# Kernel tuning notes

Measured on AMD Instinct MI355X. Metric: run time of the kernel, lower is better.

Reference implementation:

```python
import jax, jax.numpy as jnp
import numpy as np

G_DIMS = [30, 30, 24, 18, 18]
G_DOWN = [10, 10, 8, 6, 6]
S_DIM = 10
N_OBJ = 45
N_STREAMS = 5
P_DIM = sum(G_DOWN) * S_DIM          # 400
HID = 20 * S_DIM                     # 200
FREQS = np.array([0.01, 0.7, 0.91, 0.97, 0.99], dtype=np.float32)
DECAY, N_ITERS = 0.8, 5
HEB_LR, HEB_FORGET = 0.5, 0.9999
LOGSIG_RATIO, LOGSIG_OFFSET = 6.0, -2.0
B, T = 256, 8
_G_OFFS = np.concatenate([[0], np.cumsum(G_DIMS)]).astype(int)


def _leaky_clamp(x):
    # f(clamp(x, -1, 1)) with f = leaky_relu (torch default slope 0.01)
    return jax.nn.leaky_relu(jnp.clip(x, -1.0, 1.0))


def _scale_log_sigma(raw, temp=1.0):
    return LOGSIG_OFFSET + temp * jnp.tanh(raw / LOGSIG_RATIO) * LOGSIG_RATIO


def _downsample(g):  # [B, 120] -> [B, 40]; take first g_down dims of each stream
    return jnp.concatenate([g[:, o:o + d] for o, d in zip(_G_OFFS[:-1], G_DOWN)], axis=1)


def setup_inputs() -> dict:
    key = jax.random.key(0)
    ks = jax.random.split(key, 10)
    return {
        "g_seq": jax.random.normal(ks[0], (B, T, sum(G_DIMS)), jnp.float32),
        "x_idx": jax.random.randint(ks[1], (B, T), 0, N_OBJ),
        "W_comp": jax.random.normal(ks[2], (N_OBJ, S_DIM), jnp.float32) * 0.3,
        "W_repeat": jax.random.normal(ks[3], (P_DIM, sum(G_DOWN)), jnp.float32) * 0.2,
        "W_tile": jax.random.normal(ks[4], (P_DIM, N_STREAMS * S_DIM), jnp.float32) * 0.2,
        "W_tile0": jax.random.normal(ks[5], (G_DOWN[0] * S_DIM, S_DIM), jnp.float32) * 0.2,
        "w_x": jnp.ones((), jnp.float32),
        "b_x": jnp.zeros((S_DIM,), jnp.float32),
        "W1": jax.random.normal(ks[6], (S_DIM, HID), jnp.float32) * 0.2,
        "b1": jnp.zeros((HID,), jnp.float32),
        "W2": jax.random.normal(ks[7], (HID, N_OBJ), jnp.float32) * 0.1,
        "b2": jnp.zeros((N_OBJ,), jnp.float32),
        "W_lv1": jax.random.normal(ks[8], (P_DIM, P_DIM), jnp.float32) * 0.05,
        "b_lv1": jnp.zeros((P_DIM,), jnp.float32),
        "W_lv2": jax.random.normal(ks[9], (P_DIM, P_DIM), jnp.float32) * 0.05,
        "b_lv2": jnp.zeros((P_DIM,), jnp.float32),
    }


def _forward(g_seq, x_onehot, W_comp, W_repeat, W_tile, W_tile0, w_x, b_x,
             W1, b1, W2, b2, W_lv1, b_lv1, W_lv2, b_lv2):
    Bn = g_seq.shape[0]
    freqs = jnp.asarray(FREQS, dtype=g_seq.dtype)

    def step(carry, xs):
        M, x_filt = carry            # M: [B,P,P] Hebbian memory; x_filt: [B,5,10]
        g_t, x_t = xs                # g_t: [B,120], x_t: [B,45]
        # sensory compression + per-stream exponential temporal filtering
        x_c = x_t @ W_comp                                          # [B,10]
        x_filt = (1.0 - freqs)[None, :, None] * x_filt + freqs[None, :, None] * x_c[:, None, :]
        x_flat = x_filt.reshape(Bn, N_STREAMS * S_DIM)              # [B,50]
        # fused p-vector formation (_scriptable_fused_form_p)
        g_down = _downsample(g_t)                                   # [B,40]
        g_exp = g_down @ W_repeat.T                                 # [B,400]
        x_exp = x_flat @ W_tile.T                                   # [B,400]
        p_inf = _leaky_clamp(g_exp * x_exp)
        # attractor retrieval seeded from g projected to p-space (_scriptable_transform_g_to_p)
        h = _leaky_clamp(g_exp)
        for _ in range(N_ITERS):                                    # memory_iterations
            h = _leaky_clamp(DECAY * h + jnp.einsum('bij,bj->bi', M, h))
        p_ret = h
        # precision-weighted Gaussian fusion of inference and memory estimates
        lv1 = _scale_log_sigma(p_inf @ W_lv1 + b_lv1)
        lv2 = _scale_log_sigma(p_ret @ W_lv2 + b_lv2)
        inv1, inv2 = jnp.exp(-lv1), jnp.exp(-lv2)
        var_c = 1.0 / (inv1 + inv2)
        p_t = var_c * (p_inf * inv1 + p_ret * inv2)
        # Hebbian update: M <- lambda*M + eta*(p - p_hat)(p + p_hat)^T
        M = HEB_FORGET * M + HEB_LR * jnp.einsum('bi,bj->bij', p_t - p_ret, p_t + p_ret)
        # generative decode from stream-0 slice of p (GenerativeNetwork.forward_decode)
        x_s = w_x * (p_t[:, :G_DOWN[0] * S_DIM] @ W_tile0) + b_x    # [B,10]
        logits = jax.nn.elu(x_s @ W1 + b1) @ W2 + b2                # [B,45]
        return (M, x_filt), logits

    M0 = jnp.zeros((Bn, P_DIM, P_DIM), g_seq.dtype)
    xf0 = jnp.zeros((Bn, N_STREAMS, S_DIM), g_seq.dtype)
    xs = (jnp.swapaxes(g_seq, 0, 1), jnp.swapaxes(x_onehot, 0, 1))
    _, logits = jax.lax.scan(step, (M0, xf0), xs)                   # [T,B,45]
    return jnp.swapaxes(logits, 0, 1)                               # [B,T,45]


def reference(g_seq, x_idx, W_comp, W_repeat, W_tile, W_tile0, w_x, b_x,
              W1, b1, W2, b2, W_lv1, b_lv1, W_lv2, b_lv2):
    x_onehot = jax.nn.one_hot(x_idx, N_OBJ, dtype=g_seq.dtype)
    return _forward(g_seq, x_onehot, W_comp, W_repeat, W_tile, W_tile0, w_x, b_x,
                    W1, b1, W2, b2, W_lv1, b_lv1, W_lv2, b_lv2)
```

## Files before the change

kernel.cpp:

```cpp
#include <hip/hip_runtime.h>

#define kT 8
#define kG 120
#define kP 400
#define kObj 45
#define kS 10
#define kHid 200
#define NL 12
#define NV 24
#define NC (NL + NV)

__device__ __constant__ int c_gmap[40] = {
    0,1,2,3,4,5,6,7,8,9,
    30,31,32,33,34,35,36,37,38,39,
    60,61,62,63,64,65,66,67,
    84,85,86,87,88,89,
    102,103,104,105,106,107};

__device__ __constant__ float c_freq[5] = {0.01f, 0.7f, 0.91f, 0.97f, 0.99f};

__device__ __forceinline__ float leaky_clamp(float x) {
    x = fminf(fmaxf(x, -1.0f), 1.0f);
    return x > 0.0f ? x : 0.01f * x;
}

__global__ __launch_bounds__(512, 1) void tem_kernel(
    const float* __restrict__ g_seq, const int* __restrict__ x_idx,
    const float* __restrict__ W_comp, const float* __restrict__ W_repeat,
    const float* __restrict__ W_tile, const float* __restrict__ W_tile0,
    const float* __restrict__ w_x, const float* __restrict__ b_x,
    const float* __restrict__ W1, const float* __restrict__ b1,
    const float* __restrict__ W2, const float* __restrict__ b2,
    const float* __restrict__ W_lv1, const float* __restrict__ b_lv1,
    const float* __restrict__ W_lv2, const float* __restrict__ b_lv2,
    float* __restrict__ out)
{
    const int b   = blockIdx.x;
    const int tid = threadIdx.x;
    const int dim = tid;
    const bool hasD = (tid < kP);
    const int wid  = tid >> 6;
    const int lane = tid & 63;
    const int g   = tid >> 7;
    const int r   = tid & 127;
    const bool mact = (r < 100);

    const int phase = blockIdx.x >> 3;
    const int q   = (g + phase) & 3;
    const int qj0 = q * 100;
    const int soff = (phase * 2) & 63;
    const int joff = (phase * 13) % kP;

    __shared__ __align__(16) float pT[kP][kT];
    __shared__ __align__(16) float hT[kP][kT];
    __shared__ __align__(16) float lvT[kP][kT];
    __shared__ __align__(16) float xfT[50][kT];
    __shared__ __align__(16) float gdT[40][kT];
    __shared__ __align__(16) float s_wc[4][NL][kP];
    __shared__ float s_h[kP];
    __shared__ float s_u[kT][kP];
    __shared__ float s_v[kT][kP];
    __shared__ __align__(16) float s_part[4][kP];
    __shared__ float s_red[2][kT][8];
    __shared__ int   s_idx[kT];

    const float blv1 = hasD ? b_lv1[dim] : 0.0f;
    const float blv2 = hasD ? b_lv2[dim] : 0.0f;
    const float wx   = w_x[0];

    if (tid < kT) s_idx[tid] = x_idx[b * kT + tid];
    __syncthreads();

    if (mact) {
        #pragma unroll
        for (int k = 0; k < NL; ++k)
            ((float4*)&s_wc[g][k][0])[r] =
                ((const float4*)(W_lv2 + (qj0 + k) * kP))[r];
    }

    if (tid < 40) {
        int gi = c_gmap[tid];
        #pragma unroll
        for (int t = 0; t < kT; ++t)
            gdT[tid][t] = g_seq[(b * kT + t) * kG + gi];
    } else if (tid >= 64 && tid < 114) {
        int rr = tid - 64, d = rr % 10;
        float f = c_freq[rr / 10];
        float xf = 0.0f;
        #pragma unroll
        for (int t = 0; t < kT; ++t) {
            float xc = W_comp[s_idx[t] * kS + d];
            xf = (1.0f - f) * xf + f * xc;
            xfT[rr][t] = xf;
        }
    }
    __syncthreads();

    if (hasD) {
        float ge[kT], xe[kT];
        #pragma unroll
        for (int t = 0; t < kT; ++t) { ge[t] = 0.0f; xe[t] = 0.0f; }
        for (int j = 0; j < 40; ++j) {
            float w = W_repeat[dim * 40 + j];
            float4 gA = *(const float4*)&gdT[j][0];
            float4 gB = *(const float4*)&gdT[j][4];
            ge[0] += w * gA.x; ge[1] += w * gA.y; ge[2] += w * gA.z; ge[3] += w * gA.w;
            ge[4] += w * gB.x; ge[5] += w * gB.y; ge[6] += w * gB.z; ge[7] += w * gB.w;
        }
        for (int j = 0; j < 50; ++j) {
            float w = W_tile[dim * 50 + j];
            float4 xA = *(const float4*)&xfT[j][0];
            float4 xB = *(const float4*)&xfT[j][4];
            xe[0] += w * xA.x; xe[1] += w * xA.y; xe[2] += w * xA.z; xe[3] += w * xA.w;
            xe[4] += w * xB.x; xe[5] += w * xB.y; xe[6] += w * xB.z; xe[7] += w * xB.w;
        }
        float4 pA, pB, hA, hB;
        pA.x = leaky_clamp(ge[0] * xe[0]); pA.y = leaky_clamp(ge[1] * xe[1]);
        pA.z = leaky_clamp(ge[2] * xe[2]); pA.w = leaky_clamp(ge[3] * xe[3]);
        pB.x = leaky_clamp(ge[4] * xe[4]); pB.y = leaky_clamp(ge[5] * xe[5]);
        pB.z = leaky_clamp(ge[6] * xe[6]); pB.w = leaky_clamp(ge[7] * xe[7]);
        hA.x = leaky_clamp(ge[0]); hA.y = leaky_clamp(ge[1]);
        hA.z = leaky_clamp(ge[2]); hA.w = leaky_clamp(ge[3]);
        hB.x = leaky_clamp(ge[4]); hB.y = leaky_clamp(ge[5]);
        hB.z = leaky_clamp(ge[6]); hB.w = leaky_clamp(ge[7]);
        *(float4*)&pT[dim][0] = pA; *(float4*)&pT[dim][4] = pB;
        *(float4*)&hT[dim][0] = hA; *(float4*)&hT[dim][4] = hB;
    }
    __syncthreads();

    if (hasD) {
        float acc[kT];
        #pragma unroll
        for (int t = 0; t < kT; ++t) acc[t] = 0.0f;
        #pragma unroll 4
        for (int j = joff; j < kP; ++j) {
            float w = W_lv1[j * kP + dim];
            float4 pA = *(const float4*)&pT[j][0];
            float4 pB = *(const float4*)&pT[j][4];
            acc[0] += w * pA.x; acc[1] += w * pA.y; acc[2] += w * pA.z; acc[3] += w * pA.w;
            acc[4] += w * pB.x; acc[5] += w * pB.y; acc[6] += w * pB.z; acc[7] += w * pB.w;
        }
        #pragma unroll 4
        for (int j = 0; j < joff; ++j) {
            float w = W_lv1[j * kP + dim];
            float4 pA = *(const float4*)&pT[j][0];
            float4 pB = *(const float4*)&pT[j][4];
            acc[0] += w * pA.x; acc[1] += w * pA.y; acc[2] += w * pA.z; acc[3] += w * pA.w;
            acc[4] += w * pB.x; acc[5] += w * pB.y; acc[6] += w * pB.z; acc[7] += w * pB.w;
        }
        *(float4*)&lvT[dim][0] = make_float4(acc[0], acc[1], acc[2], acc[3]);
        *(float4*)&lvT[dim][4] = make_float4(acc[4], acc[5], acc[6], acc[7]);
    }
    __syncthreads();

    float4 wreg[NV];
    if (mact) {
        #pragma unroll
        for (int k = 0; k < NV; ++k)
            wreg[k] = ((const float4*)(W_lv2 + (qj0 + NL + k) * kP))[r];
    }

    int par = 0;
    for (int t = 0; t < kT; ++t) {
        float h = hasD ? hT[dim][t] : 0.0f;
        if (t == 0) {
            #pragma unroll
            for (int it = 0; it < 5; ++it) h = leaky_clamp(0.8f * h);
        } else {
            for (int it = 0; it < 5; ++it) {
                for (int s = 0; s < t; ++s) {
                    float p = hasD ? s_v[s][dim] * h : 0.0f;
                    #pragma unroll
                    for (int off = 32; off; off >>= 1) p += __shfl_down(p, off, 64);
                    if (lane == 0) s_red[par][s][wid] = p;
                }
                __syncthreads();
                if (hasD) {
                    float mh = 0.0f;
                    float c = 0.5f;
                    for (int s = t - 1; s >= 0; --s) {
                        float d = 0.0f;
                        #pragma unroll
                        for (int w = 0; w < 8; ++w) d += s_red[par][s][w];
                        mh += c * d * s_u[s][dim];
                        c *= 0.9999f;
                    }
                    h = leaky_clamp(0.8f * h + mh);
                }
                par ^= 1;
            }
        }
        if (hasD) s_h[dim] = h;
        __syncthreads();

        if (mact) {
            float4 a0{0,0,0,0}, a1{0,0,0,0}, a2{0,0,0,0}, a3{0,0,0,0};
            #pragma unroll
            for (int k = 0; k < NL; k += 4) {
                int j = qj0 + k;
                float4 w0 = ((const float4*)&s_wc[g][k+0][0])[r];
                float4 w1v = ((const float4*)&s_wc[g][k+1][0])[r];
                float4 w2v = ((const float4*)&s_wc[g][k+2][0])[r];
                float4 w3 = ((const float4*)&s_wc[g][k+3][0])[r];
                float v0 = s_h[j+0], v1 = s_h[j+1], v2 = s_h[j+2], v3 = s_h[j+3];
                a0.x += w0.x * v0; a0.y += w0.y * v0; a0.z += w0.z * v0; a0.w += w0.w * v0;
                a1.x += w1v.x * v1; a1.y += w1v.y * v1; a1.z += w1v.z * v1; a1.w += w1v.w * v1;
                a2.x += w2v.x * v2; a2.y += w2v.y * v2; a2.z += w2v.z * v2; a2.w += w2v.w * v2;
                a3.x += w3.x * v3; a3.y += w3.y * v3; a3.z += w3.z * v3; a3.w += w3.w * v3;
            }
            #pragma unroll
            for (int k = 0; k < NV; k += 4) {
                int j = qj0 + NL + k;
                float v0 = s_h[j+0], v1 = s_h[j+1], v2 = s_h[j+2], v3 = s_h[j+3];
                a0.x += wreg[k].x * v0; a0.y += wreg[k].y * v0; a0.z += wreg[k].z * v0; a0.w += wreg[k].w * v0;
                a1.x += wreg[k+1].x * v1; a1.y += wreg[k+1].y * v1; a1.z += wreg[k+1].z * v1; a1.w += wreg[k+1].w * v1;
                a2.x += wreg[k+2].x * v2; a2.y += wreg[k+2].y * v2; a2.z += wreg[k+2].z * v2; a2.w += wreg[k+2].w * v2;
                a3.x += wreg[k+3].x * v3; a3.y += wreg[k+3].y * v3; a3.z += wreg[k+3].z * v3; a3.w += wreg[k+3].w * v3;
            }
            #pragma unroll 4
            for (int jj = 0; jj < 64; jj += 2) {
                int j = qj0 + NC + ((jj + soff) & 63);
                float4 w0 = ((const float4*)(W_lv2 + (j+0) * kP))[r];
                float4 w1v = ((const float4*)(W_lv2 + (j+1) * kP))[r];
                float v0 = s_h[j+0], v1 = s_h[j+1];
                a0.x += w0.x * v0; a0.y += w0.y * v0; a0.z += w0.z * v0; a0.w += w0.w * v0;
                a1.x += w1v.x * v1; a1.y += w1v.y * v1; a1.z += w1v.z * v1; a1.w += w1v.w * v1;
            }
            float4 tot;
            tot.x = (a0.x + a1.x) + (a2.x + a3.x);
            tot.y = (a0.y + a1.y) + (a2.y + a3.y);
            tot.z = (a0.z + a1.z) + (a2.z + a3.z);
            tot.w = (a0.w + a1.w) + (a2.w + a3.w);
            ((float4*)&s_part[g][0])[r] = tot;
        }
        __syncthreads();

        if (hasD) {
            float lv2raw = (s_part[0][dim] + s_part[1][dim])
                         + (s_part[2][dim] + s_part[3][dim]) + blv2;
            float lv1raw = lvT[dim][t] + blv1;
            float l1 = -2.0f + 6.0f * tanhf(lv1raw * (1.0f / 6.0f));
            float l2 = -2.0f + 6.0f * tanhf(lv2raw * (1.0f / 6.0f));
            float i1v = expf(-l1), i2v = expf(-l2);
            float pinf = pT[dim][t];
            float p = (pinf * i1v + h * i2v) / (i1v + i2v);
            s_u[t][dim] = p - h;
            s_v[t][dim] = p + h;
        }
    }
    __syncthreads();

    float* dsc  = &hT[0][0];
    float* dhid = &lvT[0][0];

    if (tid < 480) {
        int t = tid / 60, rem = tid % 60;
        int d = rem / 6, k = rem % 6;
        int jlo = k * 17, jhi = (jlo + 17 > 100) ? 100 : jlo + 17;
        float acc = 0.0f;
        for (int j = jlo; j < jhi; ++j) {
            float pj = 0.5f * (s_u[t][j] + s_v[t][j]);
            acc += pj * W_tile0[j * kS + d];
        }
        dsc[(t * 10 + d) * 6 + k] = acc;
    }
    __syncthreads();
    if (tid < 80) {
        int t = tid / 10, d = tid % 10;
        float acc = 0.0f;
        #pragma unroll
        for (int k = 0; k < 6; ++k) acc += dsc[(t * 10 + d) * 6 + k];
        dsc[1000 + t * 10 + d] = wx * acc + b_x[d];
    }
    __syncthreads();
    for (int idx = tid; idx < kT * kHid; idx += 512) {
        int t = idx / kHid, hh = idx - t * kHid;
        float acc = b1[hh];
        #pragma unroll
        for (int d = 0; d < kS; ++d)
            acc += dsc[1000 + t * 10 + d] * W1[d * kHid + hh];
        dhid[t * kHid + hh] = acc > 0.0f ? acc : (expf(acc) - 1.0f);
    }
    __syncthreads();
    for (int idx = tid; idx < 720; idx += 512) {
        int t = idx / 90, rem = idx - t * 90;
        int half = rem / kObj, o = rem - half * kObj;
        int h0 = half * 100;
        float acc = 0.0f;
        for (int hh = h0; hh < h0 + 100; ++hh)
            acc += dhid[t * kHid + hh] * W2[hh * kObj + o];
        dsc[2000 + idx] = acc;
    }
    __syncthreads();
    if (tid < 360) {
        int t = tid / kObj, o = tid - t * kObj;
        out[(b * kT + t) * kObj + o] =
            b2[o] + dsc[2000 + t * 90 + o] + dsc[2000 + t * 90 + kObj + o];
    }
}

extern "C" void kernel_launch(void* const* d_in, const int* in_sizes, int n_in,
                              void* d_out, int out_size, void* d_ws, size_t ws_size,
                              hipStream_t stream) {
    const float* g_seq   = (const float*)d_in[0];
    const int*   x_idx   = (const int*)d_in[1];
    const float* W_comp  = (const float*)d_in[2];
    const float* W_repeat= (const float*)d_in[3];
    const float* W_tile  = (const float*)d_in[4];
    const float* W_tile0 = (const float*)d_in[5];
    const float* w_x     = (const float*)d_in[6];
    const float* b_x     = (const float*)d_in[7];
    const float* W1      = (const float*)d_in[8];
    const float* b1      = (const float*)d_in[9];
    const float* W2      = (const float*)d_in[10];
    const float* b2      = (const float*)d_in[11];
    const float* W_lv1   = (const float*)d_in[12];
    const float* b_lv1   = (const float*)d_in[13];
    const float* W_lv2   = (const float*)d_in[14];
    const float* b_lv2   = (const float*)d_in[15];
    float* out = (float*)d_out;

    const int Bn = in_sizes[0] / (kT * kG);
    tem_kernel<<<dim3(Bn), dim3(512), 0, stream>>>(
        g_seq, x_idx, W_comp, W_repeat, W_tile, W_tile0, w_x, b_x,
        W1, b1, W2, b2, W_lv1, b_lv1, W_lv2, b_lv2, out);
}
```

Before: 206.0 us.

## Double block to 1024 threads and split matvecs across more thread groups

Raises the block size from 512 to 1024 threads. The per-step W_lv2 matvec is now split over 8 row-slices of 50 rows instead of 4 slices of 100, so each thread keeps fewer cached weight rows in LDS and registers and streams a shorter tail per step. The W_lv1 precompute is split into two halves of the input dimension, combined through a shared buffer, and the decode reductions are spread over more threads. The aim is to shorten the serial per-timestep critical path with more parallel work. The cost is heavier barriers with 16 waves per block and extra partial-sum reductions.

```diff
diff --git a/kernel.cpp b/kernel.cpp
--- a/kernel.cpp
+++ b/kernel.cpp
@@ -6,9 +6,11 @@
 #define kObj 45
 #define kS 10
 #define kHid 200
-#define NL 12
-#define NV 24
-#define NC (NL + NV)
+#define NG 8
+#define SL 50
+#define NLr 4
+#define NVr 12
+#define NSr (SL - NLr - NVr)
 
 __device__ __constant__ int c_gmap[40] = {
     0,1,2,3,4,5,6,7,8,9,
@@ -24,7 +26,7 @@
     return x > 0.0f ? x : 0.01f * x;
 }
 
-__global__ __launch_bounds__(512, 1) void tem_kernel(
+__global__ __launch_bounds__(1024, 1) void tem_kernel(
     const float* __restrict__ g_seq, const int* __restrict__ x_idx,
     const float* __restrict__ W_comp, const float* __restrict__ W_repeat,
     const float* __restrict__ W_tile, const float* __restrict__ W_tile0,
@@ -41,26 +43,26 @@
     const bool hasD = (tid < kP);
     const int wid  = tid >> 6;
     const int lane = tid & 63;
-    const int g   = tid >> 7;
+    const int gg  = tid >> 7;
     const int r   = tid & 127;
     const bool mact = (r < 100);
 
     const int phase = blockIdx.x >> 3;
-    const int q   = (g + phase) & 3;
-    const int qj0 = q * 100;
-    const int soff = (phase * 2) & 63;
-    const int joff = (phase * 13) % kP;
+    const int ss  = (gg + phase) & 7;
+    const int sb  = ss * SL;
+    const int so  = phase % NSr;
+    const int joff = (phase * 13) % 200;
 
     __shared__ __align__(16) float pT[kP][kT];
     __shared__ __align__(16) float hT[kP][kT];
     __shared__ __align__(16) float lvT[kP][kT];
     __shared__ __align__(16) float xfT[50][kT];
     __shared__ __align__(16) float gdT[40][kT];
-    __shared__ __align__(16) float s_wc[4][NL][kP];
+    __shared__ __align__(16) float s_wc[NG][NLr][kP];
     __shared__ float s_h[kP];
     __shared__ float s_u[kT][kP];
     __shared__ float s_v[kT][kP];
-    __shared__ __align__(16) float s_part[4][kP];
+    __shared__ __align__(16) float s_part[NG][kP];
     __shared__ float s_red[2][kT][8];
     __shared__ int   s_idx[kT];
 
@@ -73,9 +75,9 @@
 
     if (mact) {
         #pragma unroll
-        for (int k = 0; k < NL; ++k)
-            ((float4*)&s_wc[g][k][0])[r] =
-                ((const float4*)(W_lv2 + (qj0 + k) * kP))[r];
+        for (int k = 0; k < NLr; ++k)
+            ((float4*)&s_wc[gg][k][0])[r] =
+                ((const float4*)(W_lv2 + (sb + k) * kP))[r];
     }
 
     if (tid < 40) {
@@ -128,36 +130,55 @@
     }
     __syncthreads();
 
-    if (hasD) {
+    {
+        const bool lvA = hasD;
+        const bool lvB = (tid >= 512 && tid < 912);
+        const int  ldim = lvA ? tid : (tid - 512);
         float acc[kT];
         #pragma unroll
         for (int t = 0; t < kT; ++t) acc[t] = 0.0f;
-        #pragma unroll 4
-        for (int j = joff; j < kP; ++j) {
-            float w = W_lv1[j * kP + dim];
-            float4 pA = *(const float4*)&pT[j][0];
-            float4 pB = *(const float4*)&pT[j][4];
-            acc[0] += w * pA.x; acc[1] += w * pA.y; acc[2] += w * pA.z; acc[3] += w * pA.w;
-            acc[4] += w * pB.x; acc[5] += w * pB.y; acc[6] += w * pB.z; acc[7] += w * pB.w;
-        }
-        #pragma unroll 4
-        for (int j = 0; j < joff; ++j) {
-            float w = W_lv1[j * kP + dim];
-            float4 pA = *(const float4*)&pT[j][0];
-            float4 pB = *(const float4*)&pT[j][4];
-            acc[0] += w * pA.x; acc[1] += w * pA.y; acc[2] += w * pA.z; acc[3] += w * pA.w;
-            acc[4] += w * pB.x; acc[5] += w * pB.y; acc[6] += w * pB.z; acc[7] += w * pB.w;
-        }
-        *(float4*)&lvT[dim][0] = make_float4(acc[0], acc[1], acc[2], acc[3]);
-        *(float4*)&lvT[dim][4] = make_float4(acc[4], acc[5], acc[6], acc[7]);
-    }
-    __syncthreads();
-
-    float4 wreg[NV];
+        if (lvA || lvB) {
+            const int jbase = lvA ? 0 : 200;
+            #pragma unroll 4
+            for (int jj = joff; jj < 200; ++jj) {
+                int j = jbase + jj;
+                float w = W_lv1[j * kP + ldim];
+                float4 pA = *(const float4*)&pT[j][0];
+                float4 pB = *(const float4*)&pT[j][4];
+                acc[0] += w * pA.x; acc[1] += w * pA.y; acc[2] += w * pA.z; acc[3] += w * pA.w;
+                acc[4] += w * pB.x; acc[5] += w * pB.y; acc[6] += w * pB.z; acc[7] += w * pB.w;
+            }
+            #pragma unroll 4
+            for (int jj = 0; jj < joff; ++jj) {
+                int j = jbase + jj;
+                float w = W_lv1[j * kP + ldim];
+                float4 pA = *(const float4*)&pT[j][0];
+                float4 pB = *(const float4*)&pT[j][4];
+                acc[0] += w * pA.x; acc[1] += w * pA.y; acc[2] += w * pA.z; acc[3] += w * pA.w;
+                acc[4] += w * pB.x; acc[5] += w * pB.y; acc[6] += w * pB.z; acc[7] += w * pB.w;
+            }
+        }
+        float* lv1b = &s_part[0][0];
+        if (lvB) {
+            ((float4*)lv1b)[ldim * 2 + 0] = make_float4(acc[0], acc[1], acc[2], acc[3]);
+            ((float4*)lv1b)[ldim * 2 + 1] = make_float4(acc[4], acc[5], acc[6], acc[7]);
+        }
+        __syncthreads();
+        if (hasD) {
+            float4 bA = ((float4*)lv1b)[dim * 2 + 0];
+            float4 bB = ((float4*)lv1b)[dim * 2 + 1];
+            *(float4*)&lvT[dim][0] =
+                make_float4(acc[0] + bA.x, acc[1] + bA.y, acc[2] + bA.z, acc[3] + bA.w);
+            *(float4*)&lvT[dim][4] =
+                make_float4(acc[4] + bB.x, acc[5] + bB.y, acc[6] + bB.z, acc[7] + bB.w);
+        }
+    }
+
+    float4 wreg[NVr];
     if (mact) {
         #pragma unroll
-        for (int k = 0; k < NV; ++k)
-            wreg[k] = ((const float4*)(W_lv2 + (qj0 + NL + k) * kP))[r];
+        for (int k = 0; k < NVr; ++k)
+            wreg[k] = ((const float4*)(W_lv2 + (sb + NLr + k) * kP))[r];
     }
 
     int par = 0;
@@ -168,11 +189,13 @@
             for (int it = 0; it < 5; ++it) h = leaky_clamp(0.8f * h);
         } else {
             for (int it = 0; it < 5; ++it) {
-                for (int s = 0; s < t; ++s) {
-                    float p = hasD ? s_v[s][dim] * h : 0.0f;
-                    #pragma unroll
-                    for (int off = 32; off; off >>= 1) p += __shfl_down(p, off, 64);
-                    if (lane == 0) s_red[par][s][wid] = p;
+                if (tid < 512) {
+                    for (int s = 0; s < t; ++s) {
+                        float p = hasD ? s_v[s][dim] * h : 0.0f;
+                        #pragma unroll
+                        for (int off = 32; off; off >>= 1) p += __shfl_down(p, off, 64);
+                        if (lane == 0) s_red[par][s][wid] = p;
+                    }
                 }
                 __syncthreads();
                 if (hasD) {
@@ -194,50 +217,45 @@
         __syncthreads();
 
         if (mact) {
-            float4 a0{0,0,0,0}, a1{0,0,0,0}, a2{0,0,0,0}, a3{0,0,0,0};
+            float4 a0{0,0,0,0}, a1{0,0,0,0};
             #pragma unroll
-            for (int k = 0; k < NL; k += 4) {
-                int j = qj0 + k;
-                float4 w0 = ((const float4*)&s_wc[g][k+0][0])[r];
-                float4 w1v = ((const float4*)&s_wc[g][k+1][0])[r];
-                float4 w2v = ((const float4*)&s_wc[g][k+2][0])[r];
-                float4 w3 = ((const float4*)&s_wc[g][k+3][0])[r];
-                float v0 = s_h[j+0], v1 = s_h[j+1], v2 = s_h[j+2], v3 = s_h[j+3];
+            for (int k = 0; k < NLr; k += 2) {
+                float4 w0 = ((const float4*)&s_wc[gg][k+0][0])[r];
+                float4 w1v = ((const float4*)&s_wc[gg][k+1][0])[r];
+                float v0 = s_h[sb+k+0], v1 = s_h[sb+k+1];
                 a0.x += w0.x * v0; a0.y += w0.y * v0; a0.z += w0.z * v0; a0.w += w0.w * v0;
                 a1.x += w1v.x * v1; a1.y += w1v.y * v1; a1.z += w1v.z * v1; a1.w += w1v.w * v1;
-                a2.x += w2v.x * v2; a2.y += w2v.y * v2; a2.z += w2v.z * v2; a2.w += w2v.w * v2;
-                a3.x += w3.x * v3; a3.y += w3.y * v3; a3.z += w3.z * v3; a3.w += w3.w * v3;
             }
             #pragma unroll
-            for (int k = 0; k < NV; k += 4) {
-                int j = qj0 + NL + k;
-                float v0 = s_h[j+0], v1 = s_h[j+1], v2 = s_h[j+2], v3 = s_h[j+3];
+            for (int k = 0; k < NVr; k += 2) {
+                float v0 = s_h[sb+NLr+k+0], v1 = s_h[sb+NLr+k+1];
                 a0.x += wreg[k].x * v0; a0.y += wreg[k].y * v0; a0.z += wreg[k].z * v0; a0.w += wreg[k].w * v0;
                 a1.x += wreg[k+1].x * v1; a1.y += wreg[k+1].y * v1; a1.z += wreg[k+1].z * v1; a1.w += wreg[k+1].w * v1;
-                a2.x += wreg[k+2].x * v2; a2.y += wreg[k+2].y * v2; a2.z += wreg[k+2].z * v2; a2.w += wreg[k+2].w * v2;
-                a3.x += wreg[k+3].x * v3; a3.y += wreg[k+3].y * v3; a3.z += wreg[k+3].z * v3; a3.w += wreg[k+3].w * v3;
-            }
+            }
+            const float* Wbase = W_lv2 + (sb + NLr + NVr) * kP;
             #pragma unroll 4
-            for (int jj = 0; jj < 64; jj += 2) {
-                int j = qj0 + NC + ((jj + soff) & 63);
-                float4 w0 = ((const float4*)(W_lv2 + (j+0) * kP))[r];
-                float4 w1v = ((const float4*)(W_lv2 + (j+1) * kP))[r];
-                float v0 = s_h[j+0], v1 = s_h[j+1];
+            for (int jj = 0; jj < NSr; jj += 2) {
+                int i0 = jj + so;     i0 -= (i0 >= NSr) ? NSr : 0;
+                int i1 = jj + 1 + so; i1 -= (i1 >= NSr) ? NSr : 0;
+                float4 w0 = ((const float4*)(Wbase + i0 * kP))[r];
+                float4 w1v = ((const float4*)(Wbase + i1 * kP))[r];
+                float v0 = s_h[sb + NLr + NVr + i0];
+                float v1 = s_h[sb + NLr + NVr + i1];
                 a0.x += w0.x * v0; a0.y += w0.y * v0; a0.z += w0.z * v0; a0.w += w0.w * v0;
                 a1.x += w1v.x * v1; a1.y += w1v.y * v1; a1.z += w1v.z * v1; a1.w += w1v.w * v1;
             }
             float4 tot;
-            tot.x = (a0.x + a1.x) + (a2.x + a3.x);
-            tot.y = (a0.y + a1.y) + (a2.y + a3.y);
-            tot.z = (a0.z + a1.z) + (a2.z + a3.z);
-            tot.w = (a0.w + a1.w) + (a2.w + a3.w);
-            ((float4*)&s_part[g][0])[r] = tot;
+            tot.x = a0.x + a1.x; tot.y = a0.y + a1.y;
+            tot.z = a0.z + a1.z; tot.w = a0.w + a1.w;
+            ((float4*)&s_part[gg][0])[r] = tot;
         }
         __syncthreads();
 
         if (hasD) {
-            float lv2raw = (s_part[0][dim] + s_part[1][dim])
-                         + (s_part[2][dim] + s_part[3][dim]) + blv2;
+            float lv2raw = ((s_part[0][dim] + s_part[1][dim])
+                          + (s_part[2][dim] + s_part[3][dim]))
+                         + ((s_part[4][dim] + s_part[5][dim])
+                          + (s_part[6][dim] + s_part[7][dim])) + blv2;
             float lv1raw = lvT[dim][t] + blv1;
             float l1 = -2.0f + 6.0f * tanhf(lv1raw * (1.0f / 6.0f));
             float l2 = -2.0f + 6.0f * tanhf(lv2raw * (1.0f / 6.0f));
@@ -253,43 +271,43 @@
     float* dsc  = &hT[0][0];
     float* dhid = &lvT[0][0];
 
-    if (tid < 480) {
-        int t = tid / 60, rem = tid % 60;
-        int d = rem / 6, k = rem % 6;
-        int jlo = k * 17, jhi = (jlo + 17 > 100) ? 100 : jlo + 17;
+    if (tid < 960) {
+        int t = tid / 120, rem = tid % 120;
+        int d = rem / 12, k = rem % 12;
+        int jlo = (k * 100) / 12, jhi = ((k + 1) * 100) / 12;
         float acc = 0.0f;
         for (int j = jlo; j < jhi; ++j) {
             float pj = 0.5f * (s_u[t][j] + s_v[t][j]);
             acc += pj * W_tile0[j * kS + d];
         }
-        dsc[(t * 10 + d) * 6 + k] = acc;
+        dsc[(t * 10 + d) * 12 + k] = acc;
     }
     __syncthreads();
     if (tid < 80) {
         int t = tid / 10, d = tid % 10;
         float acc = 0.0f;
         #pragma unroll
-        for (int k = 0; k < 6; ++k) acc += dsc[(t * 10 + d) * 6 + k];
-        dsc[1000 + t * 10 + d] = wx * acc + b_x[d];
-    }
-    __syncthreads();
-    for (int idx = tid; idx < kT * kHid; idx += 512) {
+        for (int k = 0; k < 12; ++k) acc += dsc[(t * 10 + d) * 12 + k];
+        dsc[1200 + t * 10 + d] = wx * acc + b_x[d];
+    }
+    __syncthreads();
+    for (int idx = tid; idx < kT * kHid; idx += 1024) {
         int t = idx / kHid, hh = idx - t * kHid;
         float acc = b1[hh];
         #pragma unroll
         for (int d = 0; d < kS; ++d)
-            acc += dsc[1000 + t * 10 + d] * W1[d * kHid + hh];
+            acc += dsc[1200 + t * 10 + d] * W1[d * kHid + hh];
         dhid[t * kHid + hh] = acc > 0.0f ? acc : (expf(acc) - 1.0f);
     }
     __syncthreads();
-    for (int idx = tid; idx < 720; idx += 512) {
-        int t = idx / 90, rem = idx - t * 90;
+    if (tid < 720) {
+        int t = tid / 90, rem = tid - t * 90;
         int half = rem / kObj, o = rem - half * kObj;
         int h0 = half * 100;
         float acc = 0.0f;
         for (int hh = h0; hh < h0 + 100; ++hh)
             acc += dhid[t * kHid + hh] * W2[hh * kObj + o];
-        dsc[2000 + idx] = acc;
+        dsc[2000 + tid] = acc;
     }
     __syncthreads();
     if (tid < 360) {
@@ -321,7 +339,7 @@
     float* out = (float*)d_out;
 
     const int Bn = in_sizes[0] / (kT * kG);
-    tem_kernel<<<dim3(Bn), dim3(512), 0, stream>>>(
+    tem_kernel<<<dim3(Bn), dim3(1024), 0, stream>>>(
         g_seq, x_idx, W_comp, W_repeat, W_tile, W_tile0, w_x, b_x,
         W1, b1, W2, b2, W_lv1, b_lv1, W_lv2, b_lv2, out);
 }
```

After: 208.7 us. No clear change (+1.3%).

## Double-buffer W_lv1 and W_lv2 streaming via async global-to-LDS loads

Applied to the files above, without the earlier changes.

Replaces direct per-thread global reads of W_lv1 and of the streamed part of W_lv2 with chunked, double-buffered async copies into LDS using global_load_lds. The persistent LDS cache of 12 W_lv2 rows is dropped, and each quarter keeps 24 rows in registers while the remaining 76 rows are staged per timestep in 13 chunks. The aim is to hide global-memory latency behind compute. In exchange it adds a block-wide barrier per chunk (25 for lv1, 13 per timestep for lv2) and a large LDS staging buffer.

```diff
diff --git a/kernel.cpp b/kernel.cpp
--- a/kernel.cpp
+++ b/kernel.cpp
@@ -6,9 +6,9 @@
 #define kObj 45
 #define kS 10
 #define kHid 200
-#define NL 12
 #define NV 24
-#define NC (NL + NV)
+#define NCH2 13
+#define NCH1 25
 
 __device__ __constant__ int c_gmap[40] = {
     0,1,2,3,4,5,6,7,8,9,
@@ -23,6 +23,23 @@
     x = fminf(fmaxf(x, -1.0f), 1.0f);
     return x > 0.0f ? x : 0.01f * x;
 }
+
+__device__ __forceinline__ void gl_lds16(const float* g, float* l) {
+    __builtin_amdgcn_global_load_lds(
+        (const __attribute__((address_space(1))) void*)g,
+        (__attribute__((address_space(3))) void*)l, 16, 0, 0);
+}
+
+__device__ __forceinline__ void stage(const float* g0, float* l0,
+                                      int nper, int lane) {
+    for (int k = 0; k < nper; k += 256) {
+        if (k + lane * 4 < nper)
+            gl_lds16(g0 + k + lane * 4, l0 + k);
+    }
+}
+
+__device__ __forceinline__ int ch_base(int c) { return c == 0 ? 0 : 4 + (c - 1) * 6; }
+__device__ __forceinline__ int ch_size(int c) { return c == 0 ? 4 : 6; }
 
 __global__ __launch_bounds__(512, 1) void tem_kernel(
     const float* __restrict__ g_seq, const int* __restrict__ x_idx,
@@ -35,34 +52,35 @@
     const float* __restrict__ W_lv2, const float* __restrict__ b_lv2,
     float* __restrict__ out)
 {
-    const int b   = blockIdx.x;
-    const int tid = threadIdx.x;
-    const int dim = tid;
+    const int b    = blockIdx.x;
+    const int tid  = threadIdx.x;
+    const int dim  = tid;
     const bool hasD = (tid < kP);
     const int wid  = tid >> 6;
+    const int widq = (tid >> 6) & 1;
     const int lane = tid & 63;
-    const int g   = tid >> 7;
-    const int r   = tid & 127;
+    const int g    = tid >> 7;
+    const int r    = tid & 127;
     const bool mact = (r < 100);
 
     const int phase = blockIdx.x >> 3;
-    const int q   = (g + phase) & 3;
-    const int qj0 = q * 100;
-    const int soff = (phase * 2) & 63;
-    const int joff = (phase * 13) % kP;
+    const int q    = (g + phase) & 3;
+    const int qj0  = q * 100;
+    const int coff  = phase % NCH2;
+    const int c1off = phase % NCH1;
 
     __shared__ __align__(16) float pT[kP][kT];
     __shared__ __align__(16) float hT[kP][kT];
     __shared__ __align__(16) float lvT[kP][kT];
     __shared__ __align__(16) float xfT[50][kT];
     __shared__ __align__(16) float gdT[40][kT];
-    __shared__ __align__(16) float s_wc[4][NL][kP];
-    __shared__ float s_h[kP];
+    __shared__ __align__(16) float s_h[kP];
     __shared__ float s_u[kT][kP];
     __shared__ float s_v[kT][kP];
     __shared__ __align__(16) float s_part[4][kP];
     __shared__ float s_red[2][kT][8];
     __shared__ int   s_idx[kT];
+    __shared__ __align__(16) float s_stg2[4][2][2400];
 
     const float blv1 = hasD ? b_lv1[dim] : 0.0f;
     const float blv2 = hasD ? b_lv2[dim] : 0.0f;
@@ -70,13 +88,6 @@
 
     if (tid < kT) s_idx[tid] = x_idx[b * kT + tid];
     __syncthreads();
-
-    if (mact) {
-        #pragma unroll
-        for (int k = 0; k < NL; ++k)
-            ((float4*)&s_wc[g][k][0])[r] =
-                ((const float4*)(W_lv2 + (qj0 + k) * kP))[r];
-    }
 
     if (tid < 40) {
         int gi = c_gmap[tid];
@@ -126,42 +137,59 @@
         *(float4*)&pT[dim][0] = pA; *(float4*)&pT[dim][4] = pB;
         *(float4*)&hT[dim][0] = hA; *(float4*)&hT[dim][4] = hB;
     }
-    __syncthreads();
-
-    if (hasD) {
+
+    float* s1 = &s_stg2[0][0][0];
+    stage(W_lv1 + c1off * 6400 + wid * 800, s1 + wid * 800, 800, lane);
+    __syncthreads();
+
+    {
         float acc[kT];
         #pragma unroll
         for (int t = 0; t < kT; ++t) acc[t] = 0.0f;
-        #pragma unroll 4
-        for (int j = joff; j < kP; ++j) {
-            float w = W_lv1[j * kP + dim];
-            float4 pA = *(const float4*)&pT[j][0];
-            float4 pB = *(const float4*)&pT[j][4];
-            acc[0] += w * pA.x; acc[1] += w * pA.y; acc[2] += w * pA.z; acc[3] += w * pA.w;
-            acc[4] += w * pB.x; acc[5] += w * pB.y; acc[6] += w * pB.z; acc[7] += w * pB.w;
-        }
-        #pragma unroll 4
-        for (int j = 0; j < joff; ++j) {
-            float w = W_lv1[j * kP + dim];
-            float4 pA = *(const float4*)&pT[j][0];
-            float4 pB = *(const float4*)&pT[j][4];
-            acc[0] += w * pA.x; acc[1] += w * pA.y; acc[2] += w * pA.z; acc[3] += w * pA.w;
-            acc[4] += w * pB.x; acc[5] += w * pB.y; acc[6] += w * pB.z; acc[7] += w * pB.w;
-        }
-        *(float4*)&lvT[dim][0] = make_float4(acc[0], acc[1], acc[2], acc[3]);
-        *(float4*)&lvT[dim][4] = make_float4(acc[4], acc[5], acc[6], acc[7]);
-    }
-    __syncthreads();
+        for (int i = 0; i < NCH1; ++i) {
+            if (i + 1 < NCH1) {
+                int cn = c1off + i + 1; if (cn >= NCH1) cn -= NCH1;
+                stage(W_lv1 + cn * 6400 + wid * 800,
+                      s1 + ((i + 1) & 1) * 6400 + wid * 800, 800, lane);
+            }
+            int cc = c1off + i; if (cc >= NCH1) cc -= NCH1;
+            if (hasD) {
+                const float* bw = s1 + (i & 1) * 6400;
+                #pragma unroll 4
+                for (int jl = 0; jl < 16; ++jl) {
+                    float w = bw[jl * 400 + dim];
+                    int j = cc * 16 + jl;
+                    float4 pA = *(const float4*)&pT[j][0];
+                    float4 pB = *(const float4*)&pT[j][4];
+                    acc[0] += w * pA.x; acc[1] += w * pA.y;
+                    acc[2] += w * pA.z; acc[3] += w * pA.w;
+                    acc[4] += w * pB.x; acc[5] += w * pB.y;
+                    acc[6] += w * pB.z; acc[7] += w * pB.w;
+                }
+            }
+            __syncthreads();
+        }
+        if (hasD) {
+            *(float4*)&lvT[dim][0] = make_float4(acc[0], acc[1], acc[2], acc[3]);
+            *(float4*)&lvT[dim][4] = make_float4(acc[4], acc[5], acc[6], acc[7]);
+        }
+    }
 
     float4 wreg[NV];
     if (mact) {
         #pragma unroll
         for (int k = 0; k < NV; ++k)
-            wreg[k] = ((const float4*)(W_lv2 + (qj0 + NL + k) * kP))[r];
+            wreg[k] = ((const float4*)(W_lv2 + (qj0 + k) * kP))[r];
     }
 
     int par = 0;
     for (int t = 0; t < kT; ++t) {
+        {
+            int sz = ch_size(coff), np = sz * 200;
+            stage(W_lv2 + (qj0 + NV + ch_base(coff)) * kP + widq * np,
+                  &s_stg2[g][0][0] + widq * np, np, lane);
+        }
+
         float h = hasD ? hT[dim][t] : 0.0f;
         if (t == 0) {
             #pragma unroll
@@ -193,51 +221,52 @@
         if (hasD) s_h[dim] = h;
         __syncthreads();
 
+        float4 aA{0,0,0,0}, aB{0,0,0,0};
         if (mact) {
-            float4 a0{0,0,0,0}, a1{0,0,0,0}, a2{0,0,0,0}, a3{0,0,0,0};
             #pragma unroll
-            for (int k = 0; k < NL; k += 4) {
-                int j = qj0 + k;
-                float4 w0 = ((const float4*)&s_wc[g][k+0][0])[r];
-                float4 w1v = ((const float4*)&s_wc[g][k+1][0])[r];
-                float4 w2v = ((const float4*)&s_wc[g][k+2][0])[r];
-                float4 w3 = ((const float4*)&s_wc[g][k+3][0])[r];
-                float v0 = s_h[j+0], v1 = s_h[j+1], v2 = s_h[j+2], v3 = s_h[j+3];
-                a0.x += w0.x * v0; a0.y += w0.y * v0; a0.z += w0.z * v0; a0.w += w0.w * v0;
-                a1.x += w1v.x * v1; a1.y += w1v.y * v1; a1.z += w1v.z * v1; a1.w += w1v.w * v1;
-                a2.x += w2v.x * v2; a2.y += w2v.y * v2; a2.z += w2v.z * v2; a2.w += w2v.w * v2;
-                a3.x += w3.x * v3; a3.y += w3.y * v3; a3.z += w3.z * v3; a3.w += w3.w * v3;
-            }
-            #pragma unroll
-            for (int k = 0; k < NV; k += 4) {
-                int j = qj0 + NL + k;
-                float v0 = s_h[j+0], v1 = s_h[j+1], v2 = s_h[j+2], v3 = s_h[j+3];
-                a0.x += wreg[k].x * v0; a0.y += wreg[k].y * v0; a0.z += wreg[k].z * v0; a0.w += wreg[k].w * v0;
-                a1.x += wreg[k+1].x * v1; a1.y += wreg[k+1].y * v1; a1.z += wreg[k+1].z * v1; a1.w += wreg[k+1].w * v1;
-                a2.x += wreg[k+2].x * v2; a2.y += wreg[k+2].y * v2; a2.z += wreg[k+2].z * v2; a2.w += wreg[k+2].w * v2;
-                a3.x += wreg[k+3].x * v3; a3.y += wreg[k+3].y * v3; a3.z += wreg[k+3].z * v3; a3.w += wreg[k+3].w * v3;
-            }
-            #pragma unroll 4
-            for (int jj = 0; jj < 64; jj += 2) {
-                int j = qj0 + NC + ((jj + soff) & 63);
-                float4 w0 = ((const float4*)(W_lv2 + (j+0) * kP))[r];
-                float4 w1v = ((const float4*)(W_lv2 + (j+1) * kP))[r];
-                float v0 = s_h[j+0], v1 = s_h[j+1];
-                a0.x += w0.x * v0; a0.y += w0.y * v0; a0.z += w0.z * v0; a0.w += w0.w * v0;
-                a1.x += w1v.x * v1; a1.y += w1v.y * v1; a1.z += w1v.z * v1; a1.w += w1v.w * v1;
-            }
-            float4 tot;
-            tot.x = (a0.x + a1.x) + (a2.x + a3.x);
-            tot.y = (a0.y + a1.y) + (a2.y + a3.y);
-            tot.z = (a0.z + a1.z) + (a2.z + a3.z);
-            tot.w = (a0.w + a1.w) + (a2.w + a3.w);
-            ((float4*)&s_part[g][0])[r] = tot;
-        }
-        __syncthreads();
+            for (int k = 0; k < NV; k += 2) {
+                float v0 = s_h[qj0 + k], v1 = s_h[qj0 + k + 1];
+                aA.x += wreg[k].x * v0; aA.y += wreg[k].y * v0;
+                aA.z += wreg[k].z * v0; aA.w += wreg[k].w * v0;
+                aB.x += wreg[k+1].x * v1; aB.y += wreg[k+1].y * v1;
+                aB.z += wreg[k+1].z * v1; aB.w += wreg[k+1].w * v1;
+            }
+        }
+        for (int i = 0; i < NCH2; ++i) {
+            if (i + 1 < NCH2) {
+                int cn = coff + i + 1; if (cn >= NCH2) cn -= NCH2;
+                int ns = ch_size(cn), np = ns * 200;
+                stage(W_lv2 + (qj0 + NV + ch_base(cn)) * kP + widq * np,
+                      &s_stg2[g][(i + 1) & 1][0] + widq * np, np, lane);
+            }
+            int cc = coff + i; if (cc >= NCH2) cc -= NCH2;
+            int cb = qj0 + NV + ch_base(cc), cs = ch_size(cc);
+            if (mact) {
+                const float* bw = &s_stg2[g][i & 1][0];
+                for (int jl = 0; jl < cs; ++jl) {
+                    float v = s_h[cb + jl];
+                    float4 w = ((const float4*)(bw + jl * 400))[r];
+                    if (jl & 1) {
+                        aB.x += w.x * v; aB.y += w.y * v;
+                        aB.z += w.z * v; aB.w += w.w * v;
+                    } else {
+                        aA.x += w.x * v; aA.y += w.y * v;
+                        aA.z += w.z * v; aA.w += w.w * v;
+                    }
+                }
+                if (i == NCH2 - 1) {
+                    float4 tot;
+                    tot.x = aA.x + aB.x; tot.y = aA.y + aB.y;
+                    tot.z = aA.z + aB.z; tot.w = aA.w + aB.w;
+                    ((float4*)&s_part[g][0])[r] = tot;
+                }
+            }
+            __syncthreads();
+        }
 
         if (hasD) {
-            float lv2raw = (s_part[0][dim] + s_part[1][dim])
-                         + (s_part[2][dim] + s_part[3][dim]) + blv2;
+            float lv2raw = ((s_part[0][dim] + s_part[1][dim])
+                          + (s_part[2][dim] + s_part[3][dim])) + blv2;
             float lv1raw = lvT[dim][t] + blv1;
             float l1 = -2.0f + 6.0f * tanhf(lv1raw * (1.0f / 6.0f));
             float l2 = -2.0f + 6.0f * tanhf(lv2raw * (1.0f / 6.0f));
```

Result: slower. 287.7 us (+39.7%).
